# Kernel tuning notes

Measured on AMD Instinct MI355X. Metric: run time of the kernel, lower is better.

The kernel has to match this reference:

```python
import jax, jax.numpy as jnp
from jax import lax
import numpy as np

B, CIN, HC, K, REC = 64, 64, 64, 3, 5
MG = 240 // REC  # 48
EPS = 1e-8


def conv2d(x, w, b, pad):
    y = lax.conv_general_dilated(x, w, (1, 1), [(pad, pad), (pad, pad)],
                                 dimension_numbers=('NCHW', 'OIHW', 'NCHW'))
    return y + b[None, :, None, None]


def conv_transpose2d(x, w, b, stride, pad):
    # PyTorch ConvTranspose2d: w is (Cin, Cout, kH, kW)
    k = w.shape[2]
    w_t = jnp.transpose(w[:, :, ::-1, ::-1], (1, 0, 2, 3))  # -> OIHW, flipped
    y = lax.conv_general_dilated(x, w_t, (1, 1),
                                 [(k - 1 - pad, k - 1 - pad)] * 2,
                                 lhs_dilation=(stride, stride),
                                 dimension_numbers=('NCHW', 'OIHW', 'NCHW'))
    return y + b[None, :, None, None]


def leaky(x):
    return jnp.where(x >= 0, x, 0.2 * x)


def setup_inputs() -> dict:
    key = jax.random.key(0)
    ks = jax.random.split(key, 12)
    s = 0.05
    return {
        'x': jax.random.normal(ks[0], (B, CIN, 64, 64), jnp.float32),
        'h': jax.random.normal(ks[1], (B, HC, 64, 64), jnp.float32),
        'c': jax.random.normal(ks[2], (B, HC, 64, 64), jnp.float32),
        'recalled_memory_feature': jax.random.normal(ks[3], (B, REC, MG, 32, 32), jnp.float32),
        'conv_w': jax.random.normal(ks[4], (5 * HC, CIN + HC, K, K), jnp.float32) * s,
        'conv_b': jax.random.normal(ks[5], (5 * HC,), jnp.float32) * s,
        'convc_w': jax.random.normal(ks[6], (MG, HC, 1, 1), jnp.float32) * s,
        'convc_b': jax.random.normal(ks[7], (MG,), jnp.float32) * s,
        'convssm_w': jax.random.normal(ks[8], (MG, MG, 4, 4), jnp.float32) * s,
        'convssm_b': jax.random.normal(ks[9], (MG,), jnp.float32) * s,
        'convfuse_w': jax.random.normal(ks[10], (HC, MG + HC, 1, 1), jnp.float32) * s,
        'convfuse_b': jax.random.normal(ks[11], (HC,), jnp.float32) * s,
    }


def reference(x, h, c, recalled_memory_feature, conv_w, conv_b, convc_w, convc_b,
              convssm_w, convssm_b, convfuse_w, convfuse_b):
    rm = recalled_memory_feature.reshape(B, REC, MG, 32, 32)
    rm_avg = rm.mean(axis=(3, 4))                      # (B, REC, MG)
    q = leaky(conv2d(c, convc_w, convc_b, 0))          # (B, MG, 64, 64)
    q_avg = q.mean(axis=(2, 3))                        # (B, MG)
    # cosine similarity along channel dim, vectorized over (B, REC)
    qn = jnp.maximum(jnp.linalg.norm(q_avg, axis=1, keepdims=True), EPS)   # (B,1)
    mn = jnp.maximum(jnp.linalg.norm(rm_avg, axis=2), EPS)                  # (B,REC)
    cos = jnp.einsum('bm,brm->br', q_avg, rm_avg) / (qn * mn)               # (B,REC)
    attn = jax.nn.softmax(cos, axis=1)                                      # (B,REC)
    mt = jnp.einsum('br,brmhw->bmhw', attn, rm)        # (B, MG, 32, 32)
    mt = leaky(conv_transpose2d(mt, convssm_w, convssm_b, 2, 1))  # (B, MG, 64, 64)

    gates = conv2d(jnp.concatenate((x, h), axis=1), conv_w, conv_b, K // 2)
    i, f, g, o, lam = jnp.split(gates, 5, axis=1)
    i = jax.nn.sigmoid(i)
    f = jax.nn.sigmoid(f)
    o = jax.nn.sigmoid(o)
    g = jnp.tanh(g)
    lam = jax.nn.sigmoid(lam)
    c_new = f * c + i * g
    h_new = o * jnp.tanh(conv2d(jnp.concatenate((c_new, mt), axis=1), convfuse_w, convfuse_b, 0))
    h_out = lam * h_new + (1.0 - lam) * h
    return (h_out, c_new)
```

## Files before the change

kernel.cpp:

```cpp
#include <hip/hip_runtime.h>
#include <hip/hip_bf16.h>
#include <cstdint>

#define HW 4096
#define MGc 48
#define RECc 5

typedef __attribute__((ext_vector_type(8))) short bf16x8;
typedef __attribute__((ext_vector_type(4))) float f32x4;

__device__ __forceinline__ float sigf(float x) { return 1.f / (1.f + expf(-x)); }
__device__ __forceinline__ float leakyf(float x) { return x >= 0.f ? x : 0.2f * x; }
__device__ __forceinline__ unsigned short f2bfu(float f) {
  __hip_bfloat16 b = __float2bfloat16(f);
  return *reinterpret_cast<unsigned short*>(&b);
}
__device__ __forceinline__ float bfu2f(unsigned short u) {
  unsigned v = ((unsigned)u) << 16;
  return __uint_as_float(v);
}
__device__ __forceinline__ void gload_lds16(const void* g, void* l) {
  __builtin_amdgcn_global_load_lds(
      (const __attribute__((address_space(1))) unsigned int*)g,
      (__attribute__((address_space(3))) unsigned int*)l, 16, 0, 0);
}

__global__ __launch_bounds__(256) void k_att(const float* __restrict__ rm,
    float* __restrict__ rm_sum, const float* __restrict__ c,
    const float* __restrict__ ccw, const float* __restrict__ ccb,
    float* __restrict__ q_part) {
  __shared__ __align__(16) char smem[13568];
  int bid = blockIdx.x, tid = threadIdx.x;
  if (bid < 15360) {
    float* sred = (float*)smem;
    int row = bid;
    const float4* p = reinterpret_cast<const float4*>(rm + (size_t)row * 1024);
    float4 v = p[tid];
    float s = v.x + v.y + v.z + v.w;
    #pragma unroll
    for (int off = 32; off; off >>= 1) s += __shfl_down(s, off);
    if ((tid & 63) == 0) sred[tid >> 6] = s;
    __syncthreads();
    if (tid == 0) rm_sum[row] = sred[0] + sred[1] + sred[2] + sred[3];
  } else {
    float* wl = (float*)smem;
    float* bl = wl + MGc * 64;
    float (*red)[MGc] = (float(*)[MGc])(bl + 64);
    int r = bid - 15360;
    int seg = r & 15, b = r >> 4;
    for (int i = tid; i < MGc * 64; i += 256) wl[i] = ccw[i];
    if (tid < MGc) bl[tid] = ccb[tid];
    __syncthreads();
    int px = seg * 256 + tid;
    float acc[MGc];
    #pragma unroll
    for (int m = 0; m < MGc; m++) acc[m] = 0.f;
    const float* cp = c + (size_t)b * 64 * HW + px;
    for (int ci = 0; ci < 64; ci++) {
      float v = cp[(size_t)ci * HW];
      #pragma unroll
      for (int m = 0; m < MGc; m++) acc[m] += wl[m * 64 + ci] * v;
    }
    int lane = tid & 63, wv = tid >> 6;
    #pragma unroll
    for (int m = 0; m < MGc; m++) {
      float t2 = leakyf(acc[m] + bl[m]);
      #pragma unroll
      for (int off = 32; off; off >>= 1) t2 += __shfl_down(t2, off);
      if (lane == 0) red[wv][m] = t2;
    }
    __syncthreads();
    if (tid < MGc) {
      float t2 = red[0][tid] + red[1][tid] + red[2][tid] + red[3][tid];
      q_part[((size_t)b * 16 + seg) * MGc + tid] = t2;
    }
  }
}

__global__ __launch_bounds__(256) void k_mid(const float* __restrict__ rm,
    const float* __restrict__ rm_sum, const float* __restrict__ q_part,
    float* __restrict__ mt_pre, const float* __restrict__ cw,
    __hip_bfloat16* __restrict__ Wp, __hip_bfloat16* __restrict__ Pp,
    const float* __restrict__ xin, const float* __restrict__ hin) {
  __shared__ __align__(16) char smem[16704];
  int bid = blockIdx.x, tid = threadIdx.x;
  if (bid < 12288) {
    float* sat = (float*)smem;
    int idx = bid * 256 + tid;
    int b = idx / (MGc * 1024);
    if (tid < 64) {
      int lane = tid;
      float q = 0.f;
      if (lane < MGc) {
        float s = 0.f;
        for (int sg = 0; sg < 16; sg++) s += q_part[((size_t)b * 16 + sg) * MGc + lane];
        q = s * (1.f / 4096.f);
      }
      float qs = q * q;
      #pragma unroll
      for (int off = 32; off; off >>= 1) qs += __shfl_xor(qs, off);
      float qn = fmaxf(sqrtf(qs), 1e-8f);
      float cosv[RECc];
      #pragma unroll
      for (int r = 0; r < RECc; r++) {
        float m = 0.f;
        if (lane < MGc) m = rm_sum[((size_t)b * RECc + r) * MGc + lane] * (1.f / 1024.f);
        float d = q * m, ms = m * m;
        #pragma unroll
        for (int off = 32; off; off >>= 1) { d += __shfl_xor(d, off); ms += __shfl_xor(ms, off); }
        float mn = fmaxf(sqrtf(ms), 1e-8f);
        cosv[r] = d / (qn * mn);
      }
      float mx = cosv[0];
      #pragma unroll
      for (int r = 1; r < RECc; r++) mx = fmaxf(mx, cosv[r]);
      float ssum = 0.f;
      #pragma unroll
      for (int r = 0; r < RECc; r++) { cosv[r] = expf(cosv[r] - mx); ssum += cosv[r]; }
      float inv = 1.f / ssum;
      #pragma unroll
      for (int r = 0; r < RECc; r++)
        if (lane == r) sat[r] = cosv[r] * inv;
    }
    __syncthreads();
    int rem = idx - b * (MGc * 1024);
    const float* base = rm + (size_t)b * RECc * MGc * 1024 + rem;
    float v = sat[0] * base[0] + sat[1] * base[MGc * 1024] + sat[2] * base[2 * MGc * 1024]
            + sat[3] * base[3 * MGc * 1024] + sat[4] * base[4 * MGc * 1024];
    mt_pre[idx] = v;
  } else if (bid < 13728) {
    int idx = (bid - 12288) * 256 + tid;
    int t = idx / (320 * 128);
    int rem = idx % (320 * 128);
    int ocp = rem / 128, ci = rem % 128;
    int nt = ocp / 80, r2 = ocp % 80, gate = r2 / 16, ml = r2 % 16;
    int oc = gate * 64 + nt * 16 + ml;
    Wp[idx] = __float2bfloat16(cw[((size_t)oc * 128 + ci) * 9 + t]);
  } else if (bid < 14768) {
    int idx = (bid - 13728) * 256 + tid;
    int b = idx / 4160, i = idx % 4160;
    bf16x8* base = reinterpret_cast<bf16x8*>(Pp);
    size_t u;
    if (i < 2112) {
      int r = (i < 1056) ? 0 : 65;
      int j = (i < 1056) ? i : i - 1056;
      u = ((size_t)b * 66 + r) * 1056 + j;
    } else {
      int i2 = i - 2112;
      int row = 1 + (i2 >> 5), k = i2 & 31;
      int px = (k < 16) ? 0 : 65, ci8 = k & 15;
      u = (((size_t)b * 66 + row) * 66 + px) * 16 + ci8;
    }
    base[u] = (bf16x8)0;
  } else {
    float (*t)[65] = (float(*)[65])smem;
    int r = bid - 14768;
    int half = r & 1, y = (r >> 1) & 63, b = r >> 7;
    const float* src = (half ? hin : xin) + (size_t)b * 64 * HW + y * 64;
    #pragma unroll
    for (int it = 0; it < 4; it++) {
      int li = it * 256 + tid;
      int ci = li >> 4, x4 = (li & 15) * 4;
      float4 v = *reinterpret_cast<const float4*>(src + (size_t)ci * HW + x4);
      t[x4][ci] = v.x; t[x4 + 1][ci] = v.y; t[x4 + 2][ci] = v.z; t[x4 + 3][ci] = v.w;
    }
    __syncthreads();
    int x = tid >> 2, c16 = (tid & 3) * 16;
    unsigned short* dst = reinterpret_cast<unsigned short*>(Pp) +
        ((((size_t)b * 66 + y + 1) * 66 + x + 1) * 128 + half * 64 + c16);
    bf16x8 o0, o1;
    #pragma unroll
    for (int j = 0; j < 8; j++) {
      o0[j] = (short)f2bfu(t[x][c16 + j]);
      o1[j] = (short)f2bfu(t[x][c16 + 8 + j]);
    }
    *reinterpret_cast<bf16x8*>(dst) = o0;
    *reinterpret_cast<bf16x8*>(dst + 8) = o1;
  }
}

__global__ __launch_bounds__(512) void k_ssm(const float* __restrict__ mt_pre,
    const float* __restrict__ w, const float* __restrict__ bias,
    __hip_bfloat16* __restrict__ mt) {
  __shared__ float in_t[12][10][20];
  __shared__ float w_t[12][48][16];
  int b = blockIdx.y;
  int tile = blockIdx.x;
  int y0 = (tile >> 1) * 16, x0 = (tile & 1) * 32;
  int wv = threadIdx.x >> 6, lane = threadIdx.x & 63;
  int co0 = wv * 6;
  int oyl = lane >> 2, xseg = lane & 3;
  int oy = y0 + oyl;
  int iy0 = (y0 >> 1) - 1, ix0 = (x0 >> 1) - 1;
  int kyA = (oy + 1) & 1;
  int iyA = (oy + 1 - kyA) >> 1;
  int rA = iyA - iy0, rB = rA - 1;
  float acc[6][8] = {};
  for (int ch = 0; ch < 4; ch++) {
    int ci0 = ch * 12;
    __syncthreads();
    for (int i = threadIdx.x; i < 12 * 10 * 18; i += 512) {
      int ci = i / 180, rr = (i % 180) / 18, cc2 = i % 18;
      int giy = iy0 + rr, gix = ix0 + cc2;
      float v = 0.f;
      if ((unsigned)giy < 32u && (unsigned)gix < 32u)
        v = mt_pre[(((size_t)b * MGc + ci0 + ci) * 32 + giy) * 32 + gix];
      in_t[ci][rr][cc2] = v;
    }
    for (int i = threadIdx.x; i < 12 * 48 * 16; i += 512)
      (&w_t[0][0][0])[i] = w[ci0 * 768 + i];
    __syncthreads();
    #pragma unroll 1
    for (int ci = 0; ci < 12; ci++) {
      float4 a0 = *reinterpret_cast<const float4*>(&in_t[ci][rA][xseg * 4]);
      float4 a1 = *reinterpret_cast<const float4*>(&in_t[ci][rA][xseg * 4 + 4]);
      float4 b0 = *reinterpret_cast<const float4*>(&in_t[ci][rB][xseg * 4]);
      float4 b1 = *reinterpret_cast<const float4*>(&in_t[ci][rB][xseg * 4 + 4]);
      float vA[6] = {a0.x, a0.y, a0.z, a0.w, a1.x, a1.y};
      float vB[6] = {b0.x, b0.y, b0.z, b0.w, b1.x, b1.y};
      #pragma unroll
      for (int co = 0; co < 6; co++) {
        const float* wp = &w_t[ci][co0 + co][0];
        float4 wA = *reinterpret_cast<const float4*>(wp + kyA * 4);
        float4 wB = *reinterpret_cast<const float4*>(wp + (kyA + 2) * 4);
        #pragma unroll
        for (int j = 0; j < 8; j++) {
          if ((j & 1) == 0) {
            int hi = (j >> 1) + 1, lo = j >> 1;
            acc[co][j] += vA[hi] * wA.y + vA[lo] * wA.w + vB[hi] * wB.y + vB[lo] * wB.w;
          } else {
            int hi = ((j + 1) >> 1) + 1, lo = (j + 1) >> 1;
            acc[co][j] += vA[hi] * wA.x + vA[lo] * wA.z + vB[hi] * wB.x + vB[lo] * wB.z;
          }
        }
      }
    }
  }
  int oxb = x0 + xseg * 8;
  #pragma unroll
  for (int co = 0; co < 6; co++) {
    float bb = bias[co0 + co];
    size_t obase = (((size_t)b * MGc + co0 + co) * 64 + oy) * 64 + oxb;
    #pragma unroll
    for (int j = 0; j < 8; j++)
      mt[obase + j] = __float2bfloat16(leakyf(acc[co][j] + bb));
  }
}

__global__ __launch_bounds__(256) void k_gates_mfma(
    const __hip_bfloat16* __restrict__ Pp, const __hip_bfloat16* __restrict__ Wp,
    const float* __restrict__ c, const float* __restrict__ cb,
    float* __restrict__ c_new, __hip_bfloat16* __restrict__ o_g,
    __hip_bfloat16* __restrict__ lam_g) {
  __shared__ bf16x8 s_in[1296];
  __shared__ bf16x8 s_w[2][960];
  int orig = blockIdx.y * gridDim.x + blockIdx.x;
  int t_id = (orig & 7) * 512 + (orig >> 3);
  int b = t_id >> 6;
  int r6 = t_id & 63;
  int ytile = r6 >> 4, xtile = (r6 >> 2) & 3, nt = r6 & 3;
  int y0 = ytile * 16, x0 = xtile * 16;
  int tid = threadIdx.x;
  int wv = tid >> 6, lane = tid & 63;
  int lane15 = lane & 15, lq = lane >> 4;

  const char* Pb = (const char*)Pp;
  const char* Wb = (const char*)Wp;

  const char* gin[6]; int din[6]; bool ain[6];
  #pragma unroll
  for (int k = 0; k < 6; k++) {
    int u = wv + 4 * k;
    int e = u * 64 + lane;
    ain[k] = (u < 21) && (e < 1296);
    int ee = (e < 1296) ? e : 0;
    int L = ee / 72, r = ee - L * 72;
    int llq = r / 18, xi = r - llq * 18;
    gin[k] = Pb + ((((size_t)b * 66 + y0 + L) * 66 + (x0 + xi)) * 256) + llq * 16;
    din[k] = ee;
  }
  const char* gwb[4]; int dwb[4]; bool awb[4];
  #pragma unroll
  for (int k = 0; k < 4; k++) {
    int u = wv + 4 * k;
    awb[k] = (u < 15);
    int uu = awb[k] ? u : 0;
    int e = uu * 64 + lane;
    int row = e / 80, ol = e - row * 80;
    int ky = row >> 2, g = row & 3;
    gwb[k] = Wb + (((size_t)(ky * 3) * 320 + nt * 80 + ol) * 128 + g * 8) * 2;
    dwb[k] = e;
  }

  f32x4 acc[4][5];
  #pragma unroll
  for (int i = 0; i < 4; i++)
    #pragma unroll
    for (int j = 0; j < 5; j++) acc[i][j] = (f32x4)0.f;

#define STAGE_W(BUF, DX, CO) do {                                                     \
    _Pragma("unroll")                                                                 \
    for (int k = 0; k < 4; k++)                                                       \
      if (awb[k]) gload_lds16(gwb[k] + (DX) * 81920 + (CO),                           \
                              (void*)&s_w[BUF][dwb[k]]);                              \
  } while (0)

#define COMP_DX(BUF, DX) do {                                                         \
    bf16x8 af[6];                                                                     \
    _Pragma("unroll")                                                                 \
    for (int r = 0; r < 6; r++)                                                       \
      af[r] = s_in[((wv * 4 + r) * 4 + lq) * 18 + lane15 + (DX)];                     \
    _Pragma("unroll")                                                                 \
    for (int ky = 0; ky < 3; ky++) {                                                  \
      bf16x8 bw[5];                                                                   \
      _Pragma("unroll")                                                               \
      for (int gg = 0; gg < 5; gg++)                                                  \
        bw[gg] = s_w[BUF][(ky * 4 + lq) * 80 + gg * 16 + lane15];                     \
      __builtin_amdgcn_s_setprio(1);                                                  \
      _Pragma("unroll")                                                               \
      for (int rr = 0; rr < 4; rr++)                                                  \
        _Pragma("unroll")                                                             \
        for (int gg = 0; gg < 5; gg++)                                                \
          acc[rr][gg] = __builtin_amdgcn_mfma_f32_16x16x32_bf16(                      \
              af[rr + ky], bw[gg], acc[rr][gg], 0, 0, 0);                             \
      __builtin_amdgcn_s_setprio(0);                                                  \
    }                                                                                 \
  } while (0)

  #pragma unroll 1
  for (int cc = 0; cc < 4; cc++) {
    int co = cc * 64;
    __syncthreads();
    #pragma unroll
    for (int k = 0; k < 6; k++)
      if (ain[k]) gload_lds16(gin[k] + co, (void*)&s_in[din[k]]);
    STAGE_W(0, 0, co);
    __syncthreads();
    STAGE_W(1, 1, co);
    COMP_DX(0, 0);
    __syncthreads();
    STAGE_W(0, 2, co);
    COMP_DX(1, 1);
    __syncthreads();
    COMP_DX(0, 2);
  }
#undef STAGE_W
#undef COMP_DX

  int m_hid = nt * 16 + lane15;
  float bi = cb[m_hid], bff = cb[64 + m_hid], bgg = cb[128 + m_hid],
        bo = cb[192 + m_hid], bl = cb[256 + m_hid];
  int xb = x0 + lq * 4;
  size_t chofs = ((size_t)b * 64 + m_hid) * HW;
  #pragma unroll
  for (int rr = 0; rr < 4; rr++) {
    int y = y0 + wv * 4 + rr;
    size_t pofs = chofs + (size_t)y * 64 + xb;
    f32x4 cold = *reinterpret_cast<const f32x4*>(c + pofs);
    f32x4 cn;
    unsigned short ov[4], lv[4];
    #pragma unroll
    for (int e = 0; e < 4; e++) {
      float i_ = sigf(acc[rr][0][e] + bi);
      float f_ = sigf(acc[rr][1][e] + bff);
      float g_ = tanhf(acc[rr][2][e] + bgg);
      float o_ = sigf(acc[rr][3][e] + bo);
      float l_ = sigf(acc[rr][4][e] + bl);
      cn[e] = f_ * cold[e] + i_ * g_;
      ov[e] = f2bfu(o_);
      lv[e] = f2bfu(l_);
    }
    *reinterpret_cast<f32x4*>(c_new + pofs) = cn;
    ushort4 ovv = {ov[0], ov[1], ov[2], ov[3]};
    ushort4 lvv = {lv[0], lv[1], lv[2], lv[3]};
    *reinterpret_cast<ushort4*>(reinterpret_cast<unsigned short*>(o_g) + pofs) = ovv;
    *reinterpret_cast<ushort4*>(reinterpret_cast<unsigned short*>(lam_g) + pofs) = lvv;
  }
}

__global__ __launch_bounds__(256) void k_fuse(const float* __restrict__ c_new,
    const __hip_bfloat16* __restrict__ mt, const __hip_bfloat16* __restrict__ o_g,
    const __hip_bfloat16* __restrict__ lam_g, const float* __restrict__ h,
    const float* __restrict__ fw, const float* __restrict__ fb,
    float* __restrict__ h_out) {
  __shared__ float wl[112][32];
  int b = blockIdx.y;
  int seg = blockIdx.x & 7, chalf = blockIdx.x >> 3;
  int co0 = chalf * 32;
  for (int i = threadIdx.x; i < 112 * 32; i += 256) {
    int ci = i >> 5, co = i & 31;
    wl[ci][co] = fw[(co0 + co) * 112 + ci];
  }
  __syncthreads();
  int px = seg * 512 + threadIdx.x * 2;
  size_t bofs = (size_t)b * 64 * HW;
  float2 acc[32];
  #pragma unroll
  for (int co = 0; co < 32; co++) { float bv = fb[co0 + co]; acc[co].x = bv; acc[co].y = bv; }
  #pragma unroll 1
  for (int ci = 0; ci < 64; ci++) {
    float2 v = *reinterpret_cast<const float2*>(c_new + bofs + (size_t)ci * HW + px);
    #pragma unroll
    for (int c4 = 0; c4 < 8; c4++) {
      float4 w = *reinterpret_cast<const float4*>(&wl[ci][c4 * 4]);
      acc[c4 * 4 + 0].x += w.x * v.x; acc[c4 * 4 + 0].y += w.x * v.y;
      acc[c4 * 4 + 1].x += w.y * v.x; acc[c4 * 4 + 1].y += w.y * v.y;
      acc[c4 * 4 + 2].x += w.z * v.x; acc[c4 * 4 + 2].y += w.z * v.y;
      acc[c4 * 4 + 3].x += w.w * v.x; acc[c4 * 4 + 3].y += w.w * v.y;
    }
  }
  const unsigned short* mtu = reinterpret_cast<const unsigned short*>(mt);
  size_t mtofs = (size_t)b * MGc * HW + px;
  #pragma unroll 1
  for (int ci = 0; ci < 48; ci++) {
    unsigned u = *reinterpret_cast<const unsigned*>(mtu + mtofs + (size_t)ci * HW);
    float vx = bfu2f((unsigned short)(u & 0xffff));
    float vy = bfu2f((unsigned short)(u >> 16));
    #pragma unroll
    for (int c4 = 0; c4 < 8; c4++) {
      float4 w = *reinterpret_cast<const float4*>(&wl[64 + ci][c4 * 4]);
      acc[c4 * 4 + 0].x += w.x * vx; acc[c4 * 4 + 0].y += w.x * vy;
      acc[c4 * 4 + 1].x += w.y * vx; acc[c4 * 4 + 1].y += w.y * vy;
      acc[c4 * 4 + 2].x += w.z * vx; acc[c4 * 4 + 2].y += w.z * vy;
      acc[c4 * 4 + 3].x += w.w * vx; acc[c4 * 4 + 3].y += w.w * vy;
    }
  }
  const unsigned short* ou = reinterpret_cast<const unsigned short*>(o_g);
  const unsigned short* lu = reinterpret_cast<const unsigned short*>(lam_g);
  #pragma unroll
  for (int co = 0; co < 32; co++) {
    size_t ofs = bofs + (size_t)(co0 + co) * HW + px;
    unsigned uo = *reinterpret_cast<const unsigned*>(ou + ofs);
    unsigned ul = *reinterpret_cast<const unsigned*>(lu + ofs);
    float2 hv = *reinterpret_cast<const float2*>(h + ofs);
    float hnx = tanhf(acc[co].x), hny = tanhf(acc[co].y);
    float ox = bfu2f((unsigned short)(uo & 0xffff)), oy = bfu2f((unsigned short)(uo >> 16));
    float lx = bfu2f((unsigned short)(ul & 0xffff)), ly = bfu2f((unsigned short)(ul >> 16));
    float2 r;
    r.x = lx * (ox * hnx) + (1.f - lx) * hv.x;
    r.y = ly * (oy * hny) + (1.f - ly) * hv.y;
    *reinterpret_cast<float2*>(h_out + ofs) = r;
  }
}

extern "C" void kernel_launch(void* const* d_in, const int* in_sizes, int n_in,
                              void* d_out, int out_size, void* d_ws, size_t ws_size,
                              hipStream_t stream) {
  const float* x   = (const float*)d_in[0];
  const float* h   = (const float*)d_in[1];
  const float* c   = (const float*)d_in[2];
  const float* rm  = (const float*)d_in[3];
  const float* cw  = (const float*)d_in[4];
  const float* cb  = (const float*)d_in[5];
  const float* ccw = (const float*)d_in[6];
  const float* ccb = (const float*)d_in[7];
  const float* sw  = (const float*)d_in[8];
  const float* sb  = (const float*)d_in[9];
  const float* fw  = (const float*)d_in[10];
  const float* fb  = (const float*)d_in[11];

  float* h_out = (float*)d_out;
  float* c_new = h_out + (size_t)16777216;

  char* ws = (char*)d_ws;
  float* rm_sum = (float*)(ws + 0);
  float* q_part = (float*)(ws + 65536);
  __hip_bfloat16* o_g   = (__hip_bfloat16*)(ws + 0);
  __hip_bfloat16* lam_g = (__hip_bfloat16*)(ws + 33554432);
  __hip_bfloat16* mt    = (__hip_bfloat16*)(ws + 67108864);
  __hip_bfloat16* Pp    = (__hip_bfloat16*)(ws + 92274688);
  __hip_bfloat16* Wp    = (__hip_bfloat16*)(ws + 163643392);
  float* mt_pre = h_out;

  k_att<<<16384, 256, 0, stream>>>(rm, rm_sum, c, ccw, ccb, q_part);
  k_mid<<<22960, 256, 0, stream>>>(rm, rm_sum, q_part, mt_pre, cw, Wp, Pp, x, h);
  k_ssm<<<dim3(8, 64), 512, 0, stream>>>(mt_pre, sw, sb, mt);
  k_gates_mfma<<<dim3(64, 64), 256, 0, stream>>>(Pp, Wp, c, cb, c_new, o_g, lam_g);
  k_fuse<<<dim3(16, 64), 256, 0, stream>>>(c_new, mt, o_g, lam_g, h, fw, fb, h_out);
}
```

Before: 629.2 us.

## Process two batch images per gates block to reuse staged weights

Each block of the gates MFMA kernel now computes two batch images at once, holding two input tiles in LDS and two accumulator sets, so each staged weight fragment is reused across both images. The grid is halved to 2048 blocks and global offsets are stored as 32-bit values. This is meant to cut weight staging traffic and LDS weight reads per MFMA. In exchange it doubles the accumulator registers (160 floats) and the input LDS footprint, which risks lower occupancy or spills despite the launch-bounds hint of two blocks.

```diff
diff --git a/kernel.cpp b/kernel.cpp
--- a/kernel.cpp
+++ b/kernel.cpp
@@ -247,16 +247,16 @@
   }
 }
 
-__global__ __launch_bounds__(256) void k_gates_mfma(
+__global__ __launch_bounds__(256, 2) void k_gates_mfma(
     const __hip_bfloat16* __restrict__ Pp, const __hip_bfloat16* __restrict__ Wp,
     const float* __restrict__ c, const float* __restrict__ cb,
     float* __restrict__ c_new, __hip_bfloat16* __restrict__ o_g,
     __hip_bfloat16* __restrict__ lam_g) {
-  __shared__ bf16x8 s_in[1296];
+  __shared__ bf16x8 s_in[2][1296];
   __shared__ bf16x8 s_w[2][960];
-  int orig = blockIdx.y * gridDim.x + blockIdx.x;
-  int t_id = (orig & 7) * 512 + (orig >> 3);
-  int b = t_id >> 6;
+  int orig = blockIdx.x;
+  int t_id = (orig & 7) * 256 + (orig >> 3);
+  int bp = t_id >> 6;
   int r6 = t_id & 63;
   int ytile = r6 >> 4, xtile = (r6 >> 2) & 3, nt = r6 & 3;
   int y0 = ytile * 16, x0 = xtile * 16;
@@ -267,7 +267,7 @@
   const char* Pb = (const char*)Pp;
   const char* Wb = (const char*)Wp;
 
-  const char* gin[6]; int din[6]; bool ain[6];
+  unsigned gin[6]; int din[6]; bool ain[6];
   #pragma unroll
   for (int k = 0; k < 6; k++) {
     int u = wv + 4 * k;
@@ -276,40 +276,54 @@
     int ee = (e < 1296) ? e : 0;
     int L = ee / 72, r = ee - L * 72;
     int llq = r / 18, xi = r - llq * 18;
-    gin[k] = Pb + ((((size_t)b * 66 + y0 + L) * 66 + (x0 + xi)) * 256) + llq * 16;
+    gin[k] = (unsigned)(((((size_t)(bp * 2) * 66 + y0 + L) * 66 + (x0 + xi)) * 256) + llq * 16);
     din[k] = ee;
   }
-  const char* gwb[4]; int dwb[4]; bool awb[4];
+  unsigned gwo[4]; int dwo[4]; bool awo[4];
   #pragma unroll
   for (int k = 0; k < 4; k++) {
     int u = wv + 4 * k;
-    awb[k] = (u < 15);
-    int uu = awb[k] ? u : 0;
+    awo[k] = (u < 15);
+    int uu = awo[k] ? u : 0;
     int e = uu * 64 + lane;
     int row = e / 80, ol = e - row * 80;
     int ky = row >> 2, g = row & 3;
-    gwb[k] = Wb + (((size_t)(ky * 3) * 320 + nt * 80 + ol) * 128 + g * 8) * 2;
-    dwb[k] = e;
-  }
-
-  f32x4 acc[4][5];
-  #pragma unroll
-  for (int i = 0; i < 4; i++)
-    #pragma unroll
-    for (int j = 0; j < 5; j++) acc[i][j] = (f32x4)0.f;
+    gwo[k] = (unsigned)((((ky * 3) * 320 + nt * 80 + ol) * 128 + g * 8) * 2);
+    dwo[k] = e;
+  }
+
+  f32x4 acc[2][4][5];
+  #pragma unroll
+  for (int bi = 0; bi < 2; bi++)
+    #pragma unroll
+    for (int i = 0; i < 4; i++)
+      #pragma unroll
+      for (int j = 0; j < 5; j++) acc[bi][i][j] = (f32x4)0.f;
+
+#define STAGE_IN(CO) do {                                                             \
+    _Pragma("unroll")                                                                 \
+    for (int k = 0; k < 6; k++)                                                       \
+      if (ain[k]) {                                                                   \
+        gload_lds16(Pb + gin[k] + (CO), (void*)&s_in[0][din[k]]);                     \
+        gload_lds16(Pb + gin[k] + 1115136 + (CO), (void*)&s_in[1][din[k]]);           \
+      }                                                                               \
+  } while (0)
 
 #define STAGE_W(BUF, DX, CO) do {                                                     \
     _Pragma("unroll")                                                                 \
     for (int k = 0; k < 4; k++)                                                       \
-      if (awb[k]) gload_lds16(gwb[k] + (DX) * 81920 + (CO),                           \
-                              (void*)&s_w[BUF][dwb[k]]);                              \
+      if (awo[k]) gload_lds16(Wb + gwo[k] + (DX) * 81920 + (CO),                      \
+                              (void*)&s_w[BUF][dwo[k]]);                              \
   } while (0)
 
 #define COMP_DX(BUF, DX) do {                                                         \
-    bf16x8 af[6];                                                                     \
+    bf16x8 af0[6], af1[6];                                                            \
     _Pragma("unroll")                                                                 \
-    for (int r = 0; r < 6; r++)                                                       \
-      af[r] = s_in[((wv * 4 + r) * 4 + lq) * 18 + lane15 + (DX)];                     \
+    for (int r = 0; r < 6; r++) {                                                     \
+      int o = ((wv * 4 + r) * 4 + lq) * 18 + lane15 + (DX);                           \
+      af0[r] = s_in[0][o];                                                            \
+      af1[r] = s_in[1][o];                                                            \
+    }                                                                                 \
     _Pragma("unroll")                                                                 \
     for (int ky = 0; ky < 3; ky++) {                                                  \
       bf16x8 bw[5];                                                                   \
@@ -320,9 +334,12 @@
       _Pragma("unroll")                                                               \
       for (int rr = 0; rr < 4; rr++)                                                  \
         _Pragma("unroll")                                                             \
-        for (int gg = 0; gg < 5; gg++)                                                \
-          acc[rr][gg] = __builtin_amdgcn_mfma_f32_16x16x32_bf16(                      \
-              af[rr + ky], bw[gg], acc[rr][gg], 0, 0, 0);                             \
+        for (int gg = 0; gg < 5; gg++) {                                              \
+          acc[0][rr][gg] = __builtin_amdgcn_mfma_f32_16x16x32_bf16(                   \
+              af0[rr + ky], bw[gg], acc[0][rr][gg], 0, 0, 0);                         \
+          acc[1][rr][gg] = __builtin_amdgcn_mfma_f32_16x16x32_bf16(                   \
+              af1[rr + ky], bw[gg], acc[1][rr][gg], 0, 0, 0);                         \
+        }                                                                             \
       __builtin_amdgcn_s_setprio(0);                                                  \
     }                                                                                 \
   } while (0)
@@ -331,9 +348,7 @@
   for (int cc = 0; cc < 4; cc++) {
     int co = cc * 64;
     __syncthreads();
-    #pragma unroll
-    for (int k = 0; k < 6; k++)
-      if (ain[k]) gload_lds16(gin[k] + co, (void*)&s_in[din[k]]);
+    STAGE_IN(co);
     STAGE_W(0, 0, co);
     __syncthreads();
     STAGE_W(1, 1, co);
@@ -344,37 +359,42 @@
     __syncthreads();
     COMP_DX(0, 2);
   }
+#undef STAGE_IN
 #undef STAGE_W
 #undef COMP_DX
 
   int m_hid = nt * 16 + lane15;
-  float bi = cb[m_hid], bff = cb[64 + m_hid], bgg = cb[128 + m_hid],
+  float bi_ = cb[m_hid], bff = cb[64 + m_hid], bgg = cb[128 + m_hid],
         bo = cb[192 + m_hid], bl = cb[256 + m_hid];
   int xb = x0 + lq * 4;
-  size_t chofs = ((size_t)b * 64 + m_hid) * HW;
-  #pragma unroll
-  for (int rr = 0; rr < 4; rr++) {
-    int y = y0 + wv * 4 + rr;
-    size_t pofs = chofs + (size_t)y * 64 + xb;
-    f32x4 cold = *reinterpret_cast<const f32x4*>(c + pofs);
-    f32x4 cn;
-    unsigned short ov[4], lv[4];
-    #pragma unroll
-    for (int e = 0; e < 4; e++) {
-      float i_ = sigf(acc[rr][0][e] + bi);
-      float f_ = sigf(acc[rr][1][e] + bff);
-      float g_ = tanhf(acc[rr][2][e] + bgg);
-      float o_ = sigf(acc[rr][3][e] + bo);
-      float l_ = sigf(acc[rr][4][e] + bl);
-      cn[e] = f_ * cold[e] + i_ * g_;
-      ov[e] = f2bfu(o_);
-      lv[e] = f2bfu(l_);
-    }
-    *reinterpret_cast<f32x4*>(c_new + pofs) = cn;
-    ushort4 ovv = {ov[0], ov[1], ov[2], ov[3]};
-    ushort4 lvv = {lv[0], lv[1], lv[2], lv[3]};
-    *reinterpret_cast<ushort4*>(reinterpret_cast<unsigned short*>(o_g) + pofs) = ovv;
-    *reinterpret_cast<ushort4*>(reinterpret_cast<unsigned short*>(lam_g) + pofs) = lvv;
+  #pragma unroll
+  for (int bi = 0; bi < 2; bi++) {
+    int b = bp * 2 + bi;
+    size_t chofs = ((size_t)b * 64 + m_hid) * HW;
+    #pragma unroll
+    for (int rr = 0; rr < 4; rr++) {
+      int y = y0 + wv * 4 + rr;
+      size_t pofs = chofs + (size_t)y * 64 + xb;
+      f32x4 cold = *reinterpret_cast<const f32x4*>(c + pofs);
+      f32x4 cn;
+      unsigned short ov[4], lv[4];
+      #pragma unroll
+      for (int e = 0; e < 4; e++) {
+        float i_ = sigf(acc[bi][rr][0][e] + bi_);
+        float f_ = sigf(acc[bi][rr][1][e] + bff);
+        float g_ = tanhf(acc[bi][rr][2][e] + bgg);
+        float o_ = sigf(acc[bi][rr][3][e] + bo);
+        float l_ = sigf(acc[bi][rr][4][e] + bl);
+        cn[e] = f_ * cold[e] + i_ * g_;
+        ov[e] = f2bfu(o_);
+        lv[e] = f2bfu(l_);
+      }
+      *reinterpret_cast<f32x4*>(c_new + pofs) = cn;
+      ushort4 ovv = {ov[0], ov[1], ov[2], ov[3]};
+      ushort4 lvv = {lv[0], lv[1], lv[2], lv[3]};
+      *reinterpret_cast<ushort4*>(reinterpret_cast<unsigned short*>(o_g) + pofs) = ovv;
+      *reinterpret_cast<ushort4*>(reinterpret_cast<unsigned short*>(lam_g) + pofs) = lvv;
+    }
   }
 }
 
@@ -475,6 +495,6 @@
   k_att<<<16384, 256, 0, stream>>>(rm, rm_sum, c, ccw, ccb, q_part);
   k_mid<<<22960, 256, 0, stream>>>(rm, rm_sum, q_part, mt_pre, cw, Wp, Pp, x, h);
   k_ssm<<<dim3(8, 64), 512, 0, stream>>>(mt_pre, sw, sb, mt);
-  k_gates_mfma<<<dim3(64, 64), 256, 0, stream>>>(Pp, Wp, c, cb, c_new, o_g, lam_g);
+  k_gates_mfma<<<2048, 256, 0, stream>>>(Pp, Wp, c, cb, c_new, o_g, lam_g);
   k_fuse<<<dim3(16, 64), 256, 0, stream>>>(c_new, mt, o_g, lam_g, h, fw, fb, h_out);
 }
```

Result: slower. 765.6 us (+21.7%).
